# Kernel tuning notes

Hardware: AMD Instinct MI355X
Metric: run time of the kernel (lower is better)

## Reference

```python
import jax, jax.numpy as jnp
import numpy as np

N_NODES = 50000
N_EDGES = 640000
DIM_IN = 128
DIM_OUT = 32
HEADS = 4
NEG_SLOPE = 0.2


def setup_inputs() -> dict:
    key = jax.random.key(0)
    ks = jax.random.split(key, 8)
    HC = HEADS * DIM_OUT
    x = jax.random.normal(ks[0], (N_NODES, DIM_IN), dtype=jnp.float32)
    edge_index = jax.random.randint(ks[1], (2, N_EDGES), 0, N_NODES, dtype=jnp.int32)
    s = 1.0 / np.sqrt(DIM_IN)
    Wl = jax.random.normal(ks[2], (DIM_IN, HC), dtype=jnp.float32) * s   # lin_l (source)
    Wr = jax.random.normal(ks[3], (DIM_IN, HC), dtype=jnp.float32) * s   # lin_r (target)
    att = jax.random.normal(ks[4], (HEADS, DIM_OUT), dtype=jnp.float32) * (1.0 / np.sqrt(DIM_OUT))
    bias = jnp.zeros((HC,), dtype=jnp.float32)
    Wp = jax.random.normal(ks[5], (HC, DIM_OUT), dtype=jnp.float32) * (1.0 / np.sqrt(HC))
    bp = jnp.zeros((DIM_OUT,), dtype=jnp.float32)
    return {"x": x, "edge_index": edge_index, "Wl": Wl, "Wr": Wr,
            "att": att, "bias": bias, "Wp": Wp, "bp": bp}


def reference(x, edge_index, Wl, Wr, att, bias, Wp, bp):
    N = x.shape[0]
    H, C = att.shape
    src = edge_index[0]  # j: message source
    dst = edge_index[1]  # i: message target (softmax segment)
    xl = (x @ Wl).reshape(N, H, C)  # source-side transform
    xr = (x @ Wr).reshape(N, H, C)  # target-side transform
    # GATv2: e_ij = a^T LeakyReLU(xl_j + xr_i)
    e = jax.nn.leaky_relu(xl[src] + xr[dst], NEG_SLOPE)        # [E,H,C]
    logits = jnp.einsum('ehc,hc->eh', e, att)                  # [E,H]
    m = jax.ops.segment_max(logits, dst, num_segments=N)       # [N,H]
    ex = jnp.exp(logits - m[dst])
    denom = jax.ops.segment_sum(ex, dst, num_segments=N)       # [N,H]
    alpha = ex / (denom[dst] + 1e-16)                          # [E,H]
    msg = xl[src] * alpha[:, :, None]                          # [E,H,C]
    out = jax.ops.segment_sum(msg, dst, num_segments=N)        # [N,H,C]
    out = out.reshape(N, H * C) + bias                         # concat heads + bias
    return out @ Wp + bp                                       # proj to dim_out
```

## Files before the change

### kernel.cpp

```cpp
#include <hip/hip_runtime.h>
#include <hip/hip_bf16.h>
#include <math.h>

#define N_NODES 50000
#define N_EDGES 640000
#define HEADS 4
#define CDIM 32
#define HC 128
#define DIN 128
#define DOUT 32
#define NEG_SLOPE 0.2f
#define TPAD 136
#define BCAP 64
#define NPB 16
#define EPT 4
#define ZERO_NB ((N_NODES + 255) / 256)
#define WT_NB (2 * DIN * HC / 256)
#define WPT_NB (DOUT * HC / 256)
#define FILL_NB (N_EDGES / (256 * EPT))
#define TF_NB ((N_NODES + 127) / 128)

typedef __hip_bfloat16 bf16;
typedef __attribute__((ext_vector_type(8))) short short8;
typedef __attribute__((ext_vector_type(4))) float floatx4;
typedef __attribute__((ext_vector_type(4))) unsigned short ushort4v;

static __device__ __forceinline__ float bflo(unsigned w) { return __uint_as_float(w << 16); }
static __device__ __forceinline__ float bfhi(unsigned w) { return __uint_as_float(w & 0xFFFF0000u); }
static __device__ __forceinline__ unsigned short f2bf(float f) {
    union { bf16 h; unsigned short u; } cv; cv.h = __float2bfloat16(f); return cv.u;
}

__global__ __launch_bounds__(256) void k_prep(
    unsigned* __restrict__ cnt,
    const float* __restrict__ Wl, const float* __restrict__ Wr,
    const float* __restrict__ bias, const float* __restrict__ Wp,
    const float* __restrict__ bp,
    bf16* __restrict__ WlF, bf16* __restrict__ WrF, bf16* __restrict__ WpT,
    float* __restrict__ cvec)
{
    const int t = threadIdx.x, b = blockIdx.x;
    if (b < ZERO_NB) {
        const int i = b * 256 + t;
        if (i < N_NODES) cnt[i] = 0u;
    } else if (b < ZERO_NB + WT_NB) {
        const int i = (b - ZERO_NB) * 256 + t;
        const int i2 = (i < DIN * HC) ? i : i - DIN * HC;
        const int c = i2 >> 7, j = i2 & 127;
        const int jt = j >> 4, m = j & 15;
        const int kk = c >> 5, quad = (c >> 3) & 3, u = c & 7;
        const int idx = (jt * 4 + kk) * 512 + (quad * 16 + m) * 8 + u;
        if (i < DIN * HC) WlF[idx] = __float2bfloat16(Wl[i2]);
        else              WrF[idx] = __float2bfloat16(Wr[i2]);
    } else if (b < ZERO_NB + WT_NB + WPT_NB) {
        const int i = (b - ZERO_NB - WT_NB) * 256 + t;
        const int c = i >> 5, j = i & 31;
        WpT[j * HC + c] = __float2bfloat16(Wp[i]);
    } else {
        __shared__ float part[8][32];
        const int j = t & 31, ch = t >> 5;
        float v = 0.f;
        for (int c = ch * 16; c < ch * 16 + 16; c++)
            v += bias[c] * Wp[c * DOUT + j];
        part[ch][j] = v;
        __syncthreads();
        if (t < 32) {
            float s = bp[t];
            #pragma unroll
            for (int k = 0; k < 8; k++) s += part[k][t];
            cvec[t] = s;
        }
    }
}

__global__ __launch_bounds__(256) void k_fill_tf(
    const int* __restrict__ ei, unsigned* __restrict__ cnt,
    unsigned short* __restrict__ srcs,
    const float* __restrict__ x,
    const bf16* __restrict__ WlF, const bf16* __restrict__ WrF,
    bf16* __restrict__ xl, bf16* __restrict__ xr)
{
    const int t = threadIdx.x, b = blockIdx.x;

    if (b < FILL_NB) {
        const int e0 = (b * 256 + t) * EPT;
        const int4 sv = *(const int4*)(ei + e0);
        const int4 dv = *(const int4*)(ei + N_EDGES + e0);
        const int s[4] = {sv.x, sv.y, sv.z, sv.w};
        const int d[4] = {dv.x, dv.y, dv.z, dv.w};
        unsigned pos[4];
        #pragma unroll
        for (int i = 0; i < EPT; i++)
            pos[i] = atomicAdd(&cnt[d[i]], 1u);
        #pragma unroll
        for (int i = 0; i < EPT; i++)
            if (pos[i] < BCAP)
                srcs[((size_t)d[i] << 6) + pos[i]] = (unsigned short)s[i];
        return;
    }

    const int n0 = (b - FILL_NB) * 128;
    const int w = t >> 6, lane = t & 63;
    const int m = lane & 15, quad = lane >> 4;
    const int na = n0 + w * 32 + m;
    const int nb = na + 16;
    const bool va = (na < N_NODES), vb = (nb < N_NODES);

    const float* xpa = x + (size_t)(va ? na : 0) * DIN;
    const float* xpb = x + (size_t)(vb ? nb : 0) * DIN;
    short8 afa[4], afb[4];
    #pragma unroll
    for (int kk = 0; kk < 4; kk++) {
        const float4 la = *(const float4*)(xpa + kk * 32 + quad * 8);
        const float4 ha = *(const float4*)(xpa + kk * 32 + quad * 8 + 4);
        const float4 lb = *(const float4*)(xpb + kk * 32 + quad * 8);
        const float4 hb = *(const float4*)(xpb + kk * 32 + quad * 8 + 4);
        short8 va8, vb8;
        va8[0] = (short)f2bf(la.x); va8[1] = (short)f2bf(la.y);
        va8[2] = (short)f2bf(la.z); va8[3] = (short)f2bf(la.w);
        va8[4] = (short)f2bf(ha.x); va8[5] = (short)f2bf(ha.y);
        va8[6] = (short)f2bf(ha.z); va8[7] = (short)f2bf(ha.w);
        vb8[0] = (short)f2bf(lb.x); vb8[1] = (short)f2bf(lb.y);
        vb8[2] = (short)f2bf(lb.z); vb8[3] = (short)f2bf(lb.w);
        vb8[4] = (short)f2bf(hb.x); vb8[5] = (short)f2bf(hb.y);
        vb8[6] = (short)f2bf(hb.z); vb8[7] = (short)f2bf(hb.w);
        afa[kk] = va8;
        afb[kk] = vb8;
    }

    const short8* wlf = (const short8*)WlF;
    const short8* wrf = (const short8*)WrF;
    #pragma unroll
    for (int jt = 0; jt < 8; jt++) {
        floatx4 aLa = {0.f,0.f,0.f,0.f}, aLb = {0.f,0.f,0.f,0.f};
        floatx4 aRa = {0.f,0.f,0.f,0.f}, aRb = {0.f,0.f,0.f,0.f};
        #pragma unroll
        for (int kk = 0; kk < 4; kk++) {
            const short8 bl = wlf[(jt * 4 + kk) * 64 + lane];
            const short8 br = wrf[(jt * 4 + kk) * 64 + lane];
            aLa = __builtin_amdgcn_mfma_f32_16x16x32_bf16(bl, afa[kk], aLa, 0, 0, 0);
            aLb = __builtin_amdgcn_mfma_f32_16x16x32_bf16(bl, afb[kk], aLb, 0, 0, 0);
            aRa = __builtin_amdgcn_mfma_f32_16x16x32_bf16(br, afa[kk], aRa, 0, 0, 0);
            aRb = __builtin_amdgcn_mfma_f32_16x16x32_bf16(br, afb[kk], aRb, 0, 0, 0);
        }
        const int joff = jt * 16 + quad * 4;
        if (va) {
            ushort4v pl, pr;
            #pragma unroll
            for (int r = 0; r < 4; r++) { pl[r] = f2bf(aLa[r]); pr[r] = f2bf(aRa[r]); }
            *(ushort4v*)(xl + (size_t)na * HC + joff) = pl;
            *(ushort4v*)(xr + (size_t)na * HC + joff) = pr;
        }
        if (vb) {
            ushort4v pl, pr;
            #pragma unroll
            for (int r = 0; r < 4; r++) { pl[r] = f2bf(aLb[r]); pr[r] = f2bf(aRb[r]); }
            *(ushort4v*)(xl + (size_t)nb * HC + joff) = pl;
            *(ushort4v*)(xr + (size_t)nb * HC + joff) = pr;
        }
    }
}

static __device__ __forceinline__ uint4 gat(
    const int srcj, const int e, const int cn,
    const unsigned* __restrict__ xl2, const int hq)
{
    const int s = __shfl(srcj, e & 63, 64);
    const size_t row = (size_t)((e < cn) ? s : 0) << 6;
    return ((const uint4*)(xl2 + row))[hq];
}

static __device__ __forceinline__ void consume_edge(
    const uint4 bx, const int eidx, const int cn,
    const float* __restrict__ xr_, const float* __restrict__ a_,
    float& s_run, float* __restrict__ acc)
{
    float x_[8];
    x_[0] = bflo(bx.x); x_[1] = bfhi(bx.x);
    x_[2] = bflo(bx.y); x_[3] = bfhi(bx.y);
    x_[4] = bflo(bx.z); x_[5] = bfhi(bx.z);
    x_[6] = bflo(bx.w); x_[7] = bfhi(bx.w);
    float p = 0.f;
    #pragma unroll
    for (int k = 0; k < 8; k++) {
        float v = x_[k] + xr_[k];
        v = fmaxf(v, NEG_SLOPE * v);
        p = fmaf(a_[k], v, p);
    }
    p += __shfl_xor(p, 1, 64);
    p += __shfl_xor(p, 2, 64);
    const float e_ = (eidx < cn) ? __expf(p) : 0.f;
    s_run += e_;
    #pragma unroll
    for (int k = 0; k < 8; k++) acc[k] = fmaf(x_[k], e_, acc[k]);
}

__global__ __launch_bounds__(256) void k_agg(
    const unsigned short* __restrict__ srcs, const unsigned* __restrict__ cnt,
    const unsigned* __restrict__ xl2,
    const unsigned* __restrict__ xr2,
    const float* __restrict__ att,
    const bf16* __restrict__ WpT,
    const float* __restrict__ cvec,
    float* __restrict__ out)
{
    __shared__ __align__(16) unsigned short srow[NPB][TPAD];
    const int t = threadIdx.x;
    const int w = t >> 6, lane = t & 63;
    const int es = lane >> 4, hq = lane & 15;

    const float4 av0 = ((const float4*)att)[hq * 2];
    const float4 av1 = ((const float4*)att)[hq * 2 + 1];
    const float a_[8] = {av0.x, av0.y, av0.z, av0.w, av1.x, av1.y, av1.z, av1.w};

    const int nb0 = blockIdx.x * NPB + w * 4;
    const uint4 cv4 = *(const uint4*)(cnt + nb0);
    int cns[4];
    cns[0] = (int)(cv4.x < 64u ? cv4.x : 64u);
    cns[1] = (int)(cv4.y < 64u ? cv4.y : 64u);
    cns[2] = (int)(cv4.z < 64u ? cv4.z : 64u);
    cns[3] = (int)(cv4.w < 64u ? cv4.w : 64u);
    int srcjv[4];
    uint4 xru[4];
    #pragma unroll
    for (int ni = 0; ni < 4; ni++) {
        srcjv[ni] = (int)srcs[((size_t)(nb0 + ni) << 6) + lane];
        xru[ni] = ((const uint4*)(xr2 + (size_t)(nb0 + ni) * 64))[hq];
    }

    #pragma unroll
    for (int ni = 0; ni < 4; ni++) {
        const int cn = cns[ni];
        float xr_[8];
        xr_[0] = bflo(xru[ni].x); xr_[1] = bfhi(xru[ni].x);
        xr_[2] = bflo(xru[ni].y); xr_[3] = bfhi(xru[ni].y);
        xr_[4] = bflo(xru[ni].z); xr_[5] = bfhi(xru[ni].z);
        xr_[6] = bflo(xru[ni].w); xr_[7] = bfhi(xru[ni].w);
        float s_run = 0.f;
        float acc[8] = {0.f, 0.f, 0.f, 0.f, 0.f, 0.f, 0.f, 0.f};
        const int sj = srcjv[ni];

        uint4 b0 = gat(sj, es,      cn, xl2, hq);
        uint4 b1 = gat(sj, es + 4,  cn, xl2, hq);
        uint4 b2 = gat(sj, es + 8,  cn, xl2, hq);
        uint4 b3 = gat(sj, es + 12, cn, xl2, hq);
        for (int i = 0; i < cn; i += 16) {
            const bool more = (i + 16 < cn);
            consume_edge(b0, i + es,      cn, xr_, a_, s_run, acc);
            if (more) b0 = gat(sj, i + 16 + es, cn, xl2, hq);
            consume_edge(b1, i + es + 4,  cn, xr_, a_, s_run, acc);
            if (more) b1 = gat(sj, i + 20 + es, cn, xl2, hq);
            consume_edge(b2, i + es + 8,  cn, xr_, a_, s_run, acc);
            if (more) b2 = gat(sj, i + 24 + es, cn, xl2, hq);
            consume_edge(b3, i + es + 12, cn, xr_, a_, s_run, acc);
            if (more) b3 = gat(sj, i + 28 + es, cn, xl2, hq);
        }
        s_run += __shfl_xor(s_run, 16, 64);
        s_run += __shfl_xor(s_run, 32, 64);
        #pragma unroll
        for (int k = 0; k < 8; k++) {
            acc[k] += __shfl_xor(acc[k], 16, 64);
            acc[k] += __shfl_xor(acc[k], 32, 64);
        }
        const float rden = 1.f / (s_run + 1e-16f);

        if (es == 0) {
            union { unsigned short s[8]; uint4 v; } pk;
            #pragma unroll
            for (int k = 0; k < 8; k++) pk.s[k] = f2bf(acc[k] * rden);
            *(uint4*)&srow[w * 4 + ni][hq * 8] = pk.v;
        }
    }
    __syncthreads();

    if (w < 2) {
        const int m = lane & 15, quad = lane >> 4;
        short8 af[4];
        #pragma unroll
        for (int kk = 0; kk < 4; kk++)
            af[kk] = *(const short8*)&srow[m][kk * 32 + quad * 8];
        floatx4 d = {0.f, 0.f, 0.f, 0.f};
        #pragma unroll
        for (int kk = 0; kk < 4; kk++) {
            const short8 bfr = *(const short8*)(WpT + (w * 16 + m) * HC + kk * 32 + quad * 8);
            d = __builtin_amdgcn_mfma_f32_16x16x32_bf16(af[kk], bfr, d, 0, 0, 0);
        }
        const int jj = w * 16 + m;
        const float cv = cvec[jj];
        #pragma unroll
        for (int r = 0; r < 4; r++) {
            const int node = blockIdx.x * NPB + quad * 4 + r;
            out[(size_t)node * DOUT + jj] = d[r] + cv;
        }
    }
}

extern "C" void kernel_launch(void* const* d_in, const int* in_sizes, int n_in,
                              void* d_out, int out_size, void* d_ws, size_t ws_size,
                              hipStream_t stream)
{
    const float* x    = (const float*)d_in[0];
    const int*   ei   = (const int*)d_in[1];
    const float* Wl   = (const float*)d_in[2];
    const float* Wr   = (const float*)d_in[3];
    const float* att  = (const float*)d_in[4];
    const float* bias = (const float*)d_in[5];
    const float* Wp   = (const float*)d_in[6];
    const float* bp   = (const float*)d_in[7];
    float* out = (float*)d_out;

    bf16* xl       = (bf16*)d_ws;
    bf16* xr       = xl + (size_t)N_NODES * HC;
    bf16* WlF      = xr + (size_t)N_NODES * HC;
    bf16* WrF      = WlF + DIN * HC;
    bf16* WpT      = WrF + DIN * HC;
    float* cvec    = (float*)(WpT + DOUT * HC);
    unsigned* cnt  = (unsigned*)(cvec + DOUT);
    unsigned short* srcs = (unsigned short*)(cnt + N_NODES);

    k_prep<<<ZERO_NB + WT_NB + WPT_NB + 1, 256, 0, stream>>>(
        cnt, Wl, Wr, bias, Wp, bp, WlF, WrF, WpT, cvec);
    k_fill_tf<<<FILL_NB + TF_NB, 256, 0, stream>>>(ei, cnt, srcs, x,
                                                   WlF, WrF, xl, xr);
    k_agg<<<N_NODES / NPB, 256, 0, stream>>>(srcs, cnt,
        (const unsigned*)xl, (const unsigned*)xr, att, WpT, cvec, out);
}
```

Measured before the change: 169.7 us.

## Fuse three kernels into one cooperative persistent kernel with grid syncs

Measured after the change: 453.8 us. 167% more time.

```diff
diff --git a/kernel.cpp b/kernel.cpp
--- a/kernel.cpp
+++ b/kernel.cpp
@@ -1,6 +1,9 @@
 #include <hip/hip_runtime.h>
+#include <hip/hip_cooperative_groups.h>
 #include <hip/hip_bf16.h>
 #include <math.h>
+
+namespace cg = cooperative_groups;
 
 #define N_NODES 50000
 #define N_EDGES 640000
@@ -17,8 +20,11 @@
 #define ZERO_NB ((N_NODES + 255) / 256)
 #define WT_NB (2 * DIN * HC / 256)
 #define WPT_NB (DOUT * HC / 256)
+#define PREP_UNITS (ZERO_NB + WT_NB + WPT_NB + 1)
 #define FILL_NB (N_EDGES / (256 * EPT))
 #define TF_NB ((N_NODES + 127) / 128)
+#define P1_UNITS (FILL_NB + TF_NB)
+#define AGG_NB (N_NODES / NPB)
 
 typedef __hip_bfloat16 bf16;
 typedef __attribute__((ext_vector_type(8))) short short8;
@@ -31,15 +37,16 @@
     union { bf16 h; unsigned short u; } cv; cv.h = __float2bfloat16(f); return cv.u;
 }
 
-__global__ __launch_bounds__(256) void k_prep(
+
+static __device__ __forceinline__ void prep_unit(
+    const int b, const int t,
     unsigned* __restrict__ cnt,
     const float* __restrict__ Wl, const float* __restrict__ Wr,
     const float* __restrict__ bias, const float* __restrict__ Wp,
     const float* __restrict__ bp,
     bf16* __restrict__ WlF, bf16* __restrict__ WrF, bf16* __restrict__ WpT,
-    float* __restrict__ cvec)
-{
-    const int t = threadIdx.x, b = blockIdx.x;
+    float* __restrict__ cvec, float (*part)[32])
+{
     if (b < ZERO_NB) {
         const int i = b * 256 + t;
         if (i < N_NODES) cnt[i] = 0u;
@@ -57,7 +64,6 @@
         const int c = i >> 5, j = i & 31;
         WpT[j * HC + c] = __float2bfloat16(Wp[i]);
     } else {
-        __shared__ float part[8][32];
         const int j = t & 31, ch = t >> 5;
         float v = 0.f;
         for (int c = ch * 16; c < ch * 16 + 16; c++)
@@ -70,36 +76,37 @@
             for (int k = 0; k < 8; k++) s += part[k][t];
             cvec[t] = s;
         }
-    }
-}
-
-__global__ __launch_bounds__(256) void k_fill_tf(
+        __syncthreads();
+    }
+}
+
+static __device__ __forceinline__ void fill_unit(
+    const int b, const int t,
     const int* __restrict__ ei, unsigned* __restrict__ cnt,
-    unsigned short* __restrict__ srcs,
+    unsigned short* __restrict__ srcs)
+{
+    const int e0 = (b * 256 + t) * EPT;
+    const int4 sv = *(const int4*)(ei + e0);
+    const int4 dv = *(const int4*)(ei + N_EDGES + e0);
+    const int s[4] = {sv.x, sv.y, sv.z, sv.w};
+    const int d[4] = {dv.x, dv.y, dv.z, dv.w};
+    unsigned pos[4];
+    #pragma unroll
+    for (int i = 0; i < EPT; i++)
+        pos[i] = atomicAdd(&cnt[d[i]], 1u);
+    #pragma unroll
+    for (int i = 0; i < EPT; i++)
+        if (pos[i] < BCAP)
+            srcs[((size_t)d[i] << 6) + pos[i]] = (unsigned short)s[i];
+}
+
+static __device__ __forceinline__ void tf_unit(
+    const int bt, const int t,
     const float* __restrict__ x,
     const bf16* __restrict__ WlF, const bf16* __restrict__ WrF,
     bf16* __restrict__ xl, bf16* __restrict__ xr)
 {
-    const int t = threadIdx.x, b = blockIdx.x;
-
-    if (b < FILL_NB) {
-        const int e0 = (b * 256 + t) * EPT;
-        const int4 sv = *(const int4*)(ei + e0);
-        const int4 dv = *(const int4*)(ei + N_EDGES + e0);
-        const int s[4] = {sv.x, sv.y, sv.z, sv.w};
-        const int d[4] = {dv.x, dv.y, dv.z, dv.w};
-        unsigned pos[4];
-        #pragma unroll
-        for (int i = 0; i < EPT; i++)
-            pos[i] = atomicAdd(&cnt[d[i]], 1u);
-        #pragma unroll
-        for (int i = 0; i < EPT; i++)
-            if (pos[i] < BCAP)
-                srcs[((size_t)d[i] << 6) + pos[i]] = (unsigned short)s[i];
-        return;
-    }
-
-    const int n0 = (b - FILL_NB) * 128;
+    const int n0 = bt * 128;
     const int w = t >> 6, lane = t & 63;
     const int m = lane & 15, quad = lane >> 4;
     const int na = n0 + w * 32 + m;
@@ -195,17 +202,13 @@
     for (int k = 0; k < 8; k++) acc[k] = fmaf(x_[k], e_, acc[k]);
 }
 
-__global__ __launch_bounds__(256) void k_agg(
+static __device__ __forceinline__ void agg_unit(
+    const int u, const int t, unsigned short (*srow)[TPAD],
     const unsigned short* __restrict__ srcs, const unsigned* __restrict__ cnt,
-    const unsigned* __restrict__ xl2,
-    const unsigned* __restrict__ xr2,
-    const float* __restrict__ att,
-    const bf16* __restrict__ WpT,
-    const float* __restrict__ cvec,
-    float* __restrict__ out)
-{
-    __shared__ __align__(16) unsigned short srow[NPB][TPAD];
-    const int t = threadIdx.x;
+    const unsigned* __restrict__ xl2, const unsigned* __restrict__ xr2,
+    const float* __restrict__ att, const bf16* __restrict__ WpT,
+    const float* __restrict__ cvec, float* __restrict__ out)
+{
     const int w = t >> 6, lane = t & 63;
     const int es = lane >> 4, hq = lane & 15;
 
@@ -213,7 +216,7 @@
     const float4 av1 = ((const float4*)att)[hq * 2 + 1];
     const float a_[8] = {av0.x, av0.y, av0.z, av0.w, av1.x, av1.y, av1.z, av1.w};
 
-    const int nb0 = blockIdx.x * NPB + w * 4;
+    const int nb0 = u * NPB + w * 4;
     const uint4 cv4 = *(const uint4*)(cnt + nb0);
     int cns[4];
     cns[0] = (int)(cv4.x < 64u ? cv4.x : 64u);
@@ -289,10 +292,80 @@
         const float cv = cvec[jj];
         #pragma unroll
         for (int r = 0; r < 4; r++) {
-            const int node = blockIdx.x * NPB + quad * 4 + r;
+            const int node = u * NPB + quad * 4 + r;
             out[(size_t)node * DOUT + jj] = d[r] + cv;
         }
     }
+    __syncthreads();
+}
+
+__global__ __launch_bounds__(256, 4) void k_main(
+    const int* __restrict__ ei, const float* __restrict__ x,
+    const float* __restrict__ Wl, const float* __restrict__ Wr,
+    const float* __restrict__ att, const float* __restrict__ bias,
+    const float* __restrict__ Wp, const float* __restrict__ bp,
+    bf16* __restrict__ WlF, bf16* __restrict__ WrF, bf16* __restrict__ WpT,
+    float* __restrict__ cvec, unsigned* __restrict__ cnt,
+    unsigned short* __restrict__ srcs,
+    bf16* __restrict__ xl, bf16* __restrict__ xr,
+    float* __restrict__ out)
+{
+    cg::grid_group grid = cg::this_grid();
+    const int t = threadIdx.x;
+    __shared__ float part[8][32];
+    __shared__ __align__(16) unsigned short srow[NPB][TPAD];
+
+    for (int b = blockIdx.x; b < PREP_UNITS; b += gridDim.x)
+        prep_unit(b, t, cnt, Wl, Wr, bias, Wp, bp, WlF, WrF, WpT, cvec, part);
+    __threadfence();
+    grid.sync();
+
+    for (int b = blockIdx.x; b < P1_UNITS; b += gridDim.x) {
+        if (b < FILL_NB) fill_unit(b, t, ei, cnt, srcs);
+        else             tf_unit(b - FILL_NB, t, x, WlF, WrF, xl, xr);
+    }
+    __threadfence();
+    grid.sync();
+
+    for (int u = blockIdx.x; u < AGG_NB; u += gridDim.x)
+        agg_unit(u, t, srow, srcs, cnt, (const unsigned*)xl,
+                 (const unsigned*)xr, att, WpT, cvec, out);
+}
+
+__global__ __launch_bounds__(256) void k_prep(
+    unsigned* __restrict__ cnt,
+    const float* __restrict__ Wl, const float* __restrict__ Wr,
+    const float* __restrict__ bias, const float* __restrict__ Wp,
+    const float* __restrict__ bp,
+    bf16* __restrict__ WlF, bf16* __restrict__ WrF, bf16* __restrict__ WpT,
+    float* __restrict__ cvec)
+{
+    __shared__ float part[8][32];
+    prep_unit(blockIdx.x, threadIdx.x, cnt, Wl, Wr, bias, Wp, bp,
+              WlF, WrF, WpT, cvec, part);
+}
+
+__global__ __launch_bounds__(256) void k_fill_tf(
+    const int* __restrict__ ei, unsigned* __restrict__ cnt,
+    unsigned short* __restrict__ srcs,
+    const float* __restrict__ x,
+    const bf16* __restrict__ WlF, const bf16* __restrict__ WrF,
+    bf16* __restrict__ xl, bf16* __restrict__ xr)
+{
+    const int b = blockIdx.x;
+    if (b < FILL_NB) fill_unit(b, threadIdx.x, ei, cnt, srcs);
+    else             tf_unit(b - FILL_NB, threadIdx.x, x, WlF, WrF, xl, xr);
+}
+
+__global__ __launch_bounds__(256) void k_agg(
+    const unsigned short* __restrict__ srcs, const unsigned* __restrict__ cnt,
+    const unsigned* __restrict__ xl2, const unsigned* __restrict__ xr2,
+    const float* __restrict__ att, const bf16* __restrict__ WpT,
+    const float* __restrict__ cvec, float* __restrict__ out)
+{
+    __shared__ __align__(16) unsigned short srow[NPB][TPAD];
+    agg_unit(blockIdx.x, threadIdx.x, srow, srcs, cnt, xl2, xr2,
+             att, WpT, cvec, out);
 }
 
 extern "C" void kernel_launch(void* const* d_in, const int* in_sizes, int n_in,
@@ -318,10 +391,44 @@
     unsigned* cnt  = (unsigned*)(cvec + DOUT);
     unsigned short* srcs = (unsigned short*)(cnt + N_NODES);
 
-    k_prep<<<ZERO_NB + WT_NB + WPT_NB + 1, 256, 0, stream>>>(
-        cnt, Wl, Wr, bias, Wp, bp, WlF, WrF, WpT, cvec);
-    k_fill_tf<<<FILL_NB + TF_NB, 256, 0, stream>>>(ei, cnt, srcs, x,
-                                                   WlF, WrF, xl, xr);
-    k_agg<<<N_NODES / NPB, 256, 0, stream>>>(srcs, cnt,
-        (const unsigned*)xl, (const unsigned*)xr, att, WpT, cvec, out);
-}
+    static int coop_grid = -2;
+    if (coop_grid == -2) {
+        coop_grid = -1;
+        int dev = 0;
+        hipDeviceProp_t prop;
+        if (hipGetDevice(&dev) == hipSuccess &&
+            hipGetDeviceProperties(&prop, dev) == hipSuccess &&
+            prop.cooperativeLaunch) {
+            int maxb = 0;
+            if (hipOccupancyMaxActiveBlocksPerMultiprocessor(
+                    &maxb, (const void*)k_main, 256, 0) == hipSuccess && maxb > 0) {
+                int g = maxb * prop.multiProcessorCount;
+                if (g > P1_UNITS) g = P1_UNITS;
+                coop_grid = g;
+            }
+        }
+    }
+
+    bool done = false;
+    if (coop_grid > 0) {
+        void* args[] = {
+            (void*)&ei, (void*)&x, (void*)&Wl, (void*)&Wr, (void*)&att,
+            (void*)&bias, (void*)&Wp, (void*)&bp,
+            (void*)&WlF, (void*)&WrF, (void*)&WpT, (void*)&cvec,
+            (void*)&cnt, (void*)&srcs, (void*)&xl, (void*)&xr, (void*)&out
+        };
+        if (hipLaunchCooperativeKernel((const void*)k_main, dim3(coop_grid),
+                                       dim3(256), args, 0, stream) == hipSuccess)
+            done = true;
+        else
+            coop_grid = -1;
+    }
+    if (!done) {
+        k_prep<<<PREP_UNITS, 256, 0, stream>>>(
+            cnt, Wl, Wr, bias, Wp, bp, WlF, WrF, WpT, cvec);
+        k_fill_tf<<<P1_UNITS, 256, 0, stream>>>(ei, cnt, srcs, x,
+                                                WlF, WrF, xl, xr);
+        k_agg<<<AGG_NB, 256, 0, stream>>>(srcs, cnt,
+            (const unsigned*)xl, (const unsigned*)xr, att, WpT, cvec, out);
+    }
+}
```
